# Performance work log

Hardware: AMD Instinct MI355X
Metric: run time of the kernel (lower is better)

The kernel has to match this reference:

```python
import jax, jax.numpy as jnp
import numpy as np

B, L, N = 128, 4096, 256
MZ_MIN, MZ_MAX = 100.0, 1000.0
STD_DEV = 0.5 * (MZ_MAX - MZ_MIN) / N  # default std_dev from __init__
THRESH_LOW_WEIGHT = -10.0


def setup_inputs() -> dict:
    key = jax.random.key(0)
    k1, k2, k3 = jax.random.split(key, 3)
    # PeakSense.__init__: means = linspace(mz_min, mz_max, n_vals) + Normal(0, 0.5*std_dev)
    mu = jnp.linspace(MZ_MIN, MZ_MAX, N, dtype=jnp.float32) \
         + (0.5 * STD_DEV) * jax.random.normal(k1, (N,), dtype=jnp.float32)
    # log_vars filled with 2*log(std_dev)
    lv = jnp.full((N,), 2.0 * float(np.log(STD_DEV)), dtype=jnp.float32)
    # spectra: masses in [mz_min, mz_max] (sorted, as real centroided spectra are), positive intensities
    masses = MZ_MIN + (MZ_MAX - MZ_MIN) * jax.random.uniform(k2, (B, L), dtype=jnp.float32)
    masses = jnp.sort(masses, axis=1)
    intensities = jax.random.uniform(k3, (B, L), dtype=jnp.float32)
    return {"mu": mu, "lv": lv, "masses": masses, "intensities": intensities}


def reference(mu, lv, masses, intensities):
    # out[b, p] = sum_i exp(-0.5*(mz[b,i]-mu[p])^2 * exp(-lv[p])) * iv[b,i],
    # where terms with arg < THRESH_LOW_WEIGHT are dropped (kernel early-exit).
    inv_s2 = jnp.exp(-lv)                                  # [N], 1/sigma^2
    d = masses[:, :, None] - mu[None, None, :]             # [B, L, N]
    arg = (-0.5) * (d * d) * inv_s2                        # [B, L, N]
    w = jnp.where(arg >= THRESH_LOW_WEIGHT, jnp.exp(arg), jnp.zeros((), arg.dtype))
    return jnp.einsum('bln,bl->bn', w, intensities)        # [B, N]
```

## Files before the change

kernel.cpp:

```cpp
#include <hip/hip_runtime.h>
#include <math.h>


#define BLOCK 256
#define SUB 4
#define PPB (BLOCK / SUB)
#define MAXL 4096
#define THRESH -10.0f

__global__ __launch_bounds__(BLOCK) void peaksense_kernel(
    const float* __restrict__ mu,
    const float* __restrict__ lv,
    const float* __restrict__ masses,
    const float* __restrict__ inten,
    float* __restrict__ out,
    int B, int L, int N)
{
    __shared__ float2 s[MAXL];

    const int pg = blockIdx.x;
    const int b  = blockIdx.y;
    const int t  = threadIdx.x;

    const float* __restrict__ mrow = masses + (size_t)b * L;
    const float* __restrict__ irow = inten  + (size_t)b * L;

    const bool fast = (L == MAXL);

    float4 m0, m1, m2, m3, i0, i1, i2, i3;
    if (fast) {
        const float4* __restrict__ mrow4 = reinterpret_cast<const float4*>(mrow);
        const float4* __restrict__ irow4 = reinterpret_cast<const float4*>(irow);
        m0 = mrow4[t];             i0 = irow4[t];
        m1 = mrow4[t +   BLOCK];   i1 = irow4[t +   BLOCK];
        m2 = mrow4[t + 2*BLOCK];   i2 = irow4[t + 2*BLOCK];
        m3 = mrow4[t + 3*BLOCK];   i3 = irow4[t + 3*BLOCK];
    } else {
        for (int i = t; i < L; i += BLOCK)
            s[i] = make_float2(mrow[i], irow[i]);
    }

    const int  lp     = t >> 2;
    const int  sub    = t & 3;
    const int  p      = pg * PPB + lp;
    const bool active = (p < N);
    const int  pc     = active ? p : (N - 1);

    const float mu_p = mu[pc];
    const float lvp  = lv[pc];
    const float inv  = __expf(-lvp);
    const float nh   = -0.5f * inv;
    const float r    = sqrtf(20.0f / inv) * 1.00001f + 1e-3f;
    const float tlo  = mu_p - r;
    const float thi  = mu_p + r;

    const bool  isHi   = sub & 1;
    const float target = isHi ? thi : tlo;
    int lo = 0, hi = L;
    while (lo < hi) {
        const int   mid = (lo + hi) >> 1;
        const float v   = mrow[mid];
        const bool  go  = isHi ? (v <= target) : (v < target);
        if (go) lo = mid + 1; else hi = mid;
    }
    const int other = __shfl_xor(lo, 1);
    const int start = isHi ? other : lo;
    const int end   = isHi ? lo    : other;

    if (fast) {
        float4* __restrict__ s4 = reinterpret_cast<float4*>(s);
        s4[2*t]                   = make_float4(m0.x, i0.x, m0.y, i0.y);
        s4[2*t + 1]               = make_float4(m0.z, i0.z, m0.w, i0.w);
        s4[2*(t +   BLOCK)]       = make_float4(m1.x, i1.x, m1.y, i1.y);
        s4[2*(t +   BLOCK) + 1]   = make_float4(m1.z, i1.z, m1.w, i1.w);
        s4[2*(t + 2*BLOCK)]       = make_float4(m2.x, i2.x, m2.y, i2.y);
        s4[2*(t + 2*BLOCK) + 1]   = make_float4(m2.z, i2.z, m2.w, i2.w);
        s4[2*(t + 3*BLOCK)]       = make_float4(m3.x, i3.x, m3.y, i3.y);
        s4[2*(t + 3*BLOCK) + 1]   = make_float4(m3.z, i3.z, m3.w, i3.w);
    }
    __syncthreads();

    float acc = 0.0f;
    for (int i = start + sub; i < end; i += SUB) {
        const float2 v  = s[i];
        const float d   = v.x - mu_p;
        const float arg = d * d * nh;
        if (arg >= THRESH)
            acc += __expf(arg) * v.y;
    }
    acc += __shfl_xor(acc, 1);
    acc += __shfl_xor(acc, 2);
    if (sub == 0 && active)
        out[(size_t)b * N + p] = acc;
}

extern "C" void kernel_launch(void* const* d_in, const int* in_sizes, int n_in,
                              void* d_out, int out_size, void* d_ws, size_t ws_size,
                              hipStream_t stream) {
    const float* mu     = (const float*)d_in[0];
    const float* lv     = (const float*)d_in[1];
    const float* masses = (const float*)d_in[2];
    const float* inten  = (const float*)d_in[3];
    float* out = (float*)d_out;

    const int N = in_sizes[0];
    const int B = out_size / N;
    const int L = in_sizes[2] / B;

    const int pgroups = (N + PPB - 1) / PPB;
    dim3 grid(pgroups, B);
    peaksense_kernel<<<grid, BLOCK, 0, stream>>>(mu, lv, masses, inten, out, B, L, N);
}
```

Measured before the change: 68.89 us.

## Use 8 lanes per peak and split shared memory into separate mass/intensity arrays

Doubles the number of threads cooperating on each peak's window from 4 to 8, which halves peaks per block and doubles the grid size. Shared memory changes from interleaved float2 to two separate float arrays, so the global-to-shared copy becomes plain float4 stores. The binary search is now done by 8 lanes where only 2 are needed, and one more shuffle stage is added. The intent is shorter per-thread loops and more parallelism, at the cost of loading each spectrum row into twice as many blocks.

```diff
diff --git a/kernel.cpp b/kernel.cpp
--- a/kernel.cpp
+++ b/kernel.cpp
@@ -3,7 +3,7 @@
 
 
 #define BLOCK 256
-#define SUB 4
+#define SUB 8
 #define PPB (BLOCK / SUB)
 #define MAXL 4096
 #define THRESH -10.0f
@@ -16,38 +16,37 @@
     float* __restrict__ out,
     int B, int L, int N)
 {
-    __shared__ float2 s[MAXL];
+    __shared__ float sm[MAXL];
+    __shared__ float si[MAXL];
 
     const int pg = blockIdx.x;
     const int b  = blockIdx.y;
     const int t  = threadIdx.x;
+
+    const int  lp     = t >> 3;
+    const int  sub    = t & 7;
+    const int  p      = pg * PPB + lp;
+    const bool active = (p < N);
+    const int  pc     = active ? p : (N - 1);
+    const float mu_p  = mu[pc];
+    const float lvp   = lv[pc];
 
     const float* __restrict__ mrow = masses + (size_t)b * L;
     const float* __restrict__ irow = inten  + (size_t)b * L;
 
     const bool fast = (L == MAXL);
 
-    float4 m0, m1, m2, m3, i0, i1, i2, i3;
+    float4 mv[4], vv[4];
     if (fast) {
-        const float4* __restrict__ mrow4 = reinterpret_cast<const float4*>(mrow);
-        const float4* __restrict__ irow4 = reinterpret_cast<const float4*>(irow);
-        m0 = mrow4[t];             i0 = irow4[t];
-        m1 = mrow4[t +   BLOCK];   i1 = irow4[t +   BLOCK];
-        m2 = mrow4[t + 2*BLOCK];   i2 = irow4[t + 2*BLOCK];
-        m3 = mrow4[t + 3*BLOCK];   i3 = irow4[t + 3*BLOCK];
-    } else {
-        for (int i = t; i < L; i += BLOCK)
-            s[i] = make_float2(mrow[i], irow[i]);
+        const float4* __restrict__ m4 = reinterpret_cast<const float4*>(mrow);
+        const float4* __restrict__ i4 = reinterpret_cast<const float4*>(irow);
+        #pragma unroll
+        for (int k = 0; k < 4; ++k) {
+            mv[k] = m4[t + k * BLOCK];
+            vv[k] = i4[t + k * BLOCK];
+        }
     }
 
-    const int  lp     = t >> 2;
-    const int  sub    = t & 3;
-    const int  p      = pg * PPB + lp;
-    const bool active = (p < N);
-    const int  pc     = active ? p : (N - 1);
-
-    const float mu_p = mu[pc];
-    const float lvp  = lv[pc];
     const float inv  = __expf(-lvp);
     const float nh   = -0.5f * inv;
     const float r    = sqrtf(20.0f / inv) * 1.00001f + 1e-3f;
@@ -68,28 +67,31 @@
     const int end   = isHi ? lo    : other;
 
     if (fast) {
-        float4* __restrict__ s4 = reinterpret_cast<float4*>(s);
-        s4[2*t]                   = make_float4(m0.x, i0.x, m0.y, i0.y);
-        s4[2*t + 1]               = make_float4(m0.z, i0.z, m0.w, i0.w);
-        s4[2*(t +   BLOCK)]       = make_float4(m1.x, i1.x, m1.y, i1.y);
-        s4[2*(t +   BLOCK) + 1]   = make_float4(m1.z, i1.z, m1.w, i1.w);
-        s4[2*(t + 2*BLOCK)]       = make_float4(m2.x, i2.x, m2.y, i2.y);
-        s4[2*(t + 2*BLOCK) + 1]   = make_float4(m2.z, i2.z, m2.w, i2.w);
-        s4[2*(t + 3*BLOCK)]       = make_float4(m3.x, i3.x, m3.y, i3.y);
-        s4[2*(t + 3*BLOCK) + 1]   = make_float4(m3.z, i3.z, m3.w, i3.w);
+        float4* __restrict__ smw = reinterpret_cast<float4*>(sm);
+        float4* __restrict__ siw = reinterpret_cast<float4*>(si);
+        #pragma unroll
+        for (int k = 0; k < 4; ++k) {
+            smw[t + k * BLOCK] = mv[k];
+            siw[t + k * BLOCK] = vv[k];
+        }
+    } else {
+        for (int i = t; i < L; i += BLOCK) {
+            sm[i] = mrow[i];
+            si[i] = irow[i];
+        }
     }
     __syncthreads();
 
     float acc = 0.0f;
     for (int i = start + sub; i < end; i += SUB) {
-        const float2 v  = s[i];
-        const float d   = v.x - mu_p;
+        const float d   = sm[i] - mu_p;
         const float arg = d * d * nh;
         if (arg >= THRESH)
-            acc += __expf(arg) * v.y;
+            acc += __expf(arg) * si[i];
     }
     acc += __shfl_xor(acc, 1);
     acc += __shfl_xor(acc, 2);
+    acc += __shfl_xor(acc, 4);
     if (sub == 0 && active)
         out[(size_t)b * N + p] = acc;
 }
```

Result: slower. 78.82 us (+14.4%).
